# Kernel optimization log

Hardware: AMD Instinct MI355X
Metric: run time of the kernel (lower is better)

## Reference

```python
import jax, jax.numpy as jnp
import numpy as np

N_NODES = 100000


def _degrees(src, dst):
    ones = jnp.ones(src.shape[0], dtype=jnp.float32)
    out_deg = jax.ops.segment_sum(ones, src, num_segments=N_NODES)
    in_deg = jax.ops.segment_sum(ones, dst, num_segments=N_NODES)
    # DGL clamps degrees to a minimum of 1 before the power
    inv_sqrt_out = jax.lax.rsqrt(jnp.maximum(out_deg, 1.0))
    inv_sqrt_in = jax.lax.rsqrt(jnp.maximum(in_deg, 1.0))
    return inv_sqrt_out, inv_sqrt_in


def _graph_conv(h, W, b, src, dst, inv_sqrt_out, inv_sqrt_in):
    # DGL GraphConv, norm='both': D_out^{-1/2} on src feats, SpMM-sum, D_in^{-1/2} on dst
    h = h * inv_sqrt_out[:, None]
    h = h @ W  # applying weight before aggregation is mathematically identical
    agg = jax.ops.segment_sum(h[src], dst, num_segments=N_NODES)
    return agg * inv_sqrt_in[:, None] + b


def setup_inputs() -> dict:
    key = jax.random.key(0)
    ks = jax.random.split(key, 6)
    E, IN, HID = 1600000, 128, 128
    scale = 1.0 / np.sqrt(IN)
    return {
        "feat": jax.random.normal(ks[0], (N_NODES, IN), dtype=jnp.float32),
        "W0": jax.random.normal(ks[1], (IN, HID), dtype=jnp.float32) * scale,
        "b0": jnp.zeros((HID,), dtype=jnp.float32),
        "W1": jax.random.normal(ks[2], (HID, HID), dtype=jnp.float32) * scale,
        "b1": jnp.zeros((HID,), dtype=jnp.float32),
        "W2": jax.random.normal(ks[3], (HID, HID), dtype=jnp.float32) * scale,
        "b2": jnp.zeros((HID,), dtype=jnp.float32),
        "src": jax.random.randint(ks[4], (E,), 0, N_NODES, dtype=jnp.int32),
        "dst": jax.random.randint(ks[5], (E,), 0, N_NODES, dtype=jnp.int32),
    }


def reference(feat, W0, b0, W1, b1, W2, b2, src, dst):
    inv_sqrt_out, inv_sqrt_in = _degrees(src, dst)
    skips = [feat]
    h = feat
    for W, b in ((W0, b0), (W1, b1), (W2, b2)):
        h = jax.nn.relu(_graph_conv(h, W, b, src, dst, inv_sqrt_out, inv_sqrt_in))
        skips.append(h)
    return jnp.concatenate(skips, axis=1)  # torch.hstack on 2D == concat along dim 1
```

## Files before the change

kernel.cpp:

```cpp
#include <hip/hip_runtime.h>
#include <hip/hip_fp16.h>

#define NN 100000
#define NE 1600000
#define FD 128
#define OS 512
#define LDA 136
#define NBKT 196
#define PCH 4096

typedef __attribute__((ext_vector_type(8))) short short8;
typedef __attribute__((ext_vector_type(4))) float f32x4;

__device__ __forceinline__ short f2bf(float x) {
    unsigned u = __float_as_uint(x);
    u = (u + 0x7fff + ((u >> 16) & 1)) >> 16;
    return (short)u;
}

__global__ void k_init_out(const float* __restrict__ feat, float* __restrict__ out) {
    const size_t total = (size_t)NN * 32;
    for (size_t i = (size_t)blockIdx.x * blockDim.x + threadIdx.x; i < total;
         i += (size_t)gridDim.x * blockDim.x) {
        size_t n = i >> 5;
        int c4 = (int)(i & 31);
        ((float4*)(out + n * OS))[c4] = ((const float4*)feat)[n * 32 + c4];
    }
}

__global__ void k_prep_w(const float* __restrict__ W0, const float* __restrict__ W1,
                         const float* __restrict__ W2, short* __restrict__ Wt) {
    int i = blockIdx.x * blockDim.x + threadIdx.x;
    if (i >= 3 * FD * FD) return;
    int l = i >> 14, r = i & (FD * FD - 1);
    int n = r >> 7, k = r & 127;
    const float* W = (l == 0) ? W0 : ((l == 1) ? W1 : W2);
    Wt[i] = f2bf(W[k * FD + n]);
}

__global__ __launch_bounds__(256) void k_deg(const int* __restrict__ src,
                                             const int* __restrict__ dst,
                                             int* __restrict__ cnt_out,
                                             int* __restrict__ bktcnt) {
    __shared__ int h[NBKT];
    for (int i = threadIdx.x; i < NBKT; i += 256) h[i] = 0;
    __syncthreads();
    const int total4 = NE / 4;
    for (int i = blockIdx.x * blockDim.x + threadIdx.x; i < total4;
         i += gridDim.x * blockDim.x) {
        int4 s = ((const int4*)src)[i];
        int4 d = ((const int4*)dst)[i];
        atomicAdd(&cnt_out[s.x], 1); atomicAdd(&cnt_out[s.y], 1);
        atomicAdd(&cnt_out[s.z], 1); atomicAdd(&cnt_out[s.w], 1);
        atomicAdd(&h[d.x >> 9], 1); atomicAdd(&h[d.y >> 9], 1);
        atomicAdd(&h[d.z >> 9], 1); atomicAdd(&h[d.w >> 9], 1);
    }
    __syncthreads();
    for (int i = threadIdx.x; i < NBKT; i += 256)
        if (h[i]) atomicAdd(&bktcnt[i], h[i]);
}

__global__ void k_invsqrt(const int* __restrict__ cnt, float* __restrict__ inv, int n) {
    int i = blockIdx.x * blockDim.x + threadIdx.x;
    if (i < n) inv[i] = rsqrtf((float)max(cnt[i], 1));
}

__global__ __launch_bounds__(256) void k_bkt_scan(const int* __restrict__ bktcnt,
                                                  int* __restrict__ bkt_base,
                                                  int* __restrict__ bkt_cursor) {
    __shared__ int s[256];
    const int tid = threadIdx.x;
    int v = (tid < NBKT) ? bktcnt[tid] : 0;
    s[tid] = v;
    __syncthreads();
    for (int off = 1; off < 256; off <<= 1) {
        int t = (tid >= off) ? s[tid - off] : 0;
        __syncthreads();
        s[tid] += t;
        __syncthreads();
    }
    int excl = s[tid] - v;
    if (tid < NBKT) { bkt_base[tid] = excl; bkt_cursor[tid] = excl; }
    if (tid == NBKT - 1) bkt_base[NBKT] = excl + v;
}

__global__ __launch_bounds__(256) void k_part(const int* __restrict__ src,
                                              const int* __restrict__ dst,
                                              int* __restrict__ bkt_cursor,
                                              int2* __restrict__ pairs) {
    __shared__ int hist[NBKT];
    __shared__ int base[NBKT];
    __shared__ int lofs[NBKT];
    const int tid = threadIdx.x;
    const int e0 = blockIdx.x * PCH;
    for (int i = tid; i < NBKT; i += 256) { hist[i] = 0; lofs[i] = 0; }
    __syncthreads();
    int md[16], ms[16];
    #pragma unroll
    for (int k = 0; k < 16; ++k) {
        int e = e0 + k * 256 + tid;
        md[k] = (e < NE) ? dst[e] : -1;
        ms[k] = (e < NE) ? src[e] : 0;
    }
    #pragma unroll
    for (int k = 0; k < 16; ++k)
        if (md[k] >= 0) atomicAdd(&hist[md[k] >> 9], 1);
    __syncthreads();
    for (int i = tid; i < NBKT; i += 256)
        base[i] = hist[i] ? atomicAdd(&bkt_cursor[i], hist[i]) : 0;
    __syncthreads();
    #pragma unroll
    for (int k = 0; k < 16; ++k)
        if (md[k] >= 0) {
            int b = md[k] >> 9;
            int off = atomicAdd(&lofs[b], 1);
            pairs[base[b] + off] = make_int2(ms[k], md[k]);
        }
}

__global__ __launch_bounds__(256) void k_build(const int2* __restrict__ pairs,
                                               const int* __restrict__ bkt_base,
                                               int* __restrict__ row_ptr,
                                               int* __restrict__ col,
                                               float* __restrict__ inv_in) {
    __shared__ int cnt_s[512];
    __shared__ int wsum[4];
    const int b = blockIdx.x;
    const int tid = threadIdx.x;
    const int lane = tid & 63, wid = tid >> 6;
    const int ebeg = bkt_base[b], eend = bkt_base[b + 1];
    const int n0 = b << 9;
    cnt_s[tid] = 0; cnt_s[tid + 256] = 0;
    __syncthreads();
    for (int e = ebeg + tid; e < eend; e += 256)
        atomicAdd(&cnt_s[pairs[e].y - n0], 1);
    __syncthreads();
    const int v0 = cnt_s[2 * tid], v1 = cnt_s[2 * tid + 1];
    const int sum2 = v0 + v1;
    int incl = sum2;
    #pragma unroll
    for (int off = 1; off < 64; off <<= 1) {
        int t = __shfl_up(incl, off, 64);
        if (lane >= off) incl += t;
    }
    if (lane == 63) wsum[wid] = incl;
    __syncthreads();
    if (tid == 0) {
        int c = 0;
        #pragma unroll
        for (int i = 0; i < 4; ++i) { int t = wsum[i]; wsum[i] = c; c += t; }
    }
    __syncthreads();
    const int e0 = wsum[wid] + incl - sum2;
    cnt_s[2 * tid] = e0;
    cnt_s[2 * tid + 1] = e0 + v0;
    const int g0 = n0 + 2 * tid, g1 = g0 + 1;
    if (g0 < NN) { row_ptr[g0] = ebeg + e0; inv_in[g0] = rsqrtf((float)max(v0, 1)); }
    if (g1 < NN) { row_ptr[g1] = ebeg + e0 + v0; inv_in[g1] = rsqrtf((float)max(v1, 1)); }
    if (b == NBKT - 1 && tid == 0) row_ptr[NN] = eend;
    __syncthreads();
    for (int e = ebeg + tid; e < eend; e += 256) {
        int2 p = pairs[e];
        int pos = atomicAdd(&cnt_s[p.y - n0], 1);
        col[ebeg + pos] = p.x;
    }
}

__global__ __launch_bounds__(256) void k_gemm(const float* __restrict__ h, int hstride,
                                              const short* __restrict__ Wt,
                                              const float* __restrict__ inv_out,
                                              unsigned char* __restrict__ tmp8,
                                              float* __restrict__ scales) {
    __shared__ short Ws[FD * LDA];
    __shared__ short hA[64 * LDA];
    const int tid = threadIdx.x;
    for (int i = tid; i < FD * 16; i += 256) {
        int n = i >> 4, c = i & 15;
        short8 v = *(const short8*)(Wt + n * FD + c * 8);
        *(short8*)(&Ws[n * LDA + c * 8]) = v;
    }
    const int row0 = blockIdx.x * 128;
    const int wid = tid >> 6, lane = tid & 63;
    const int m = lane & 15, quad = lane >> 4;

    for (int sub = 0; sub < 2; ++sub) {
        const int rbase = row0 + sub * 64;
        __syncthreads();
        for (int i = tid; i < 64 * 32; i += 256) {
            int r = i >> 5, c4 = i & 31;
            int gr = rbase + r;
            float4 v = make_float4(0.f, 0.f, 0.f, 0.f);
            if (gr < NN) v = ((const float4*)(h + (size_t)gr * hstride))[c4];
            short4 b;
            b.x = f2bf(v.x); b.y = f2bf(v.y); b.z = f2bf(v.z); b.w = f2bf(v.w);
            *(short4*)(&hA[r * LDA + c4 * 4]) = b;
        }
        __syncthreads();
        const int rtile = rbase + wid * 16;
        short8 a0 = *(const short8*)(&hA[(wid * 16 + m) * LDA + 0 * 32 + quad * 8]);
        short8 a1 = *(const short8*)(&hA[(wid * 16 + m) * LDA + 1 * 32 + quad * 8]);
        short8 a2 = *(const short8*)(&hA[(wid * 16 + m) * LDA + 2 * 32 + quad * 8]);
        short8 a3 = *(const short8*)(&hA[(wid * 16 + m) * LDA + 3 * 32 + quad * 8]);
        float s0, s1, s2, s3;
        {
            int r = rtile + quad * 4;
            s0 = (r + 0 < NN) ? inv_out[r + 0] : 0.f;
            s1 = (r + 1 < NN) ? inv_out[r + 1] : 0.f;
            s2 = (r + 2 < NN) ? inv_out[r + 2] : 0.f;
            s3 = (r + 3 < NN) ? inv_out[r + 3] : 0.f;
        }
        f32x4 accs[8];
        #pragma unroll
        for (int ct = 0; ct < 8; ++ct) {
            f32x4 acc = {0.f, 0.f, 0.f, 0.f};
            short8 b0 = *(const short8*)(&Ws[(ct * 16 + m) * LDA + 0 * 32 + quad * 8]);
            short8 b1 = *(const short8*)(&Ws[(ct * 16 + m) * LDA + 1 * 32 + quad * 8]);
            short8 b2 = *(const short8*)(&Ws[(ct * 16 + m) * LDA + 2 * 32 + quad * 8]);
            short8 b3 = *(const short8*)(&Ws[(ct * 16 + m) * LDA + 3 * 32 + quad * 8]);
            acc = __builtin_amdgcn_mfma_f32_16x16x32_bf16(a0, b0, acc, 0, 0, 0);
            acc = __builtin_amdgcn_mfma_f32_16x16x32_bf16(a1, b1, acc, 0, 0, 0);
            acc = __builtin_amdgcn_mfma_f32_16x16x32_bf16(a2, b2, acc, 0, 0, 0);
            acc = __builtin_amdgcn_mfma_f32_16x16x32_bf16(a3, b3, acc, 0, 0, 0);
            acc[0] *= s0; acc[1] *= s1; acc[2] *= s2; acc[3] *= s3;
            accs[ct] = acc;
        }
        float pm0 = 0.f, pm1 = 0.f, pm2 = 0.f, pm3 = 0.f;
        #pragma unroll
        for (int ct = 0; ct < 8; ++ct) {
            pm0 = fmaxf(pm0, fabsf(accs[ct][0]));
            pm1 = fmaxf(pm1, fabsf(accs[ct][1]));
            pm2 = fmaxf(pm2, fabsf(accs[ct][2]));
            pm3 = fmaxf(pm3, fabsf(accs[ct][3]));
        }
        #pragma unroll
        for (int off = 1; off < 16; off <<= 1) {
            pm0 = fmaxf(pm0, __shfl_xor(pm0, off));
            pm1 = fmaxf(pm1, __shfl_xor(pm1, off));
            pm2 = fmaxf(pm2, __shfl_xor(pm2, off));
            pm3 = fmaxf(pm3, __shfl_xor(pm3, off));
        }
        const float is0 = pm0 > 0.f ? 127.f / pm0 : 0.f;
        const float is1 = pm1 > 0.f ? 127.f / pm1 : 0.f;
        const float is2 = pm2 > 0.f ? 127.f / pm2 : 0.f;
        const float is3 = pm3 > 0.f ? 127.f / pm3 : 0.f;
        const int r = rtile + quad * 4;
        if (m == 0) {
            const float inv127 = 1.f / 127.f;
            if (r + 3 < NN) {
                float4 sv = make_float4(pm0 * inv127, pm1 * inv127, pm2 * inv127, pm3 * inv127);
                *((float4*)(scales + r)) = sv;
            } else {
                if (r + 0 < NN) scales[r + 0] = pm0 * inv127;
                if (r + 1 < NN) scales[r + 1] = pm1 * inv127;
                if (r + 2 < NN) scales[r + 2] = pm2 * inv127;
                if (r + 3 < NN) scales[r + 3] = pm3 * inv127;
            }
        }
        unsigned long long w0 = 0ull, w1 = 0ull, w2 = 0ull, w3 = 0ull;
        #pragma unroll
        for (int ct = 0; ct < 8; ++ct) {
            unsigned char q0 = (unsigned char)(char)(int)rintf(accs[ct][0] * is0);
            unsigned char q1 = (unsigned char)(char)(int)rintf(accs[ct][1] * is1);
            unsigned char q2 = (unsigned char)(char)(int)rintf(accs[ct][2] * is2);
            unsigned char q3 = (unsigned char)(char)(int)rintf(accs[ct][3] * is3);
            w0 |= (unsigned long long)q0 << (8 * ct);
            w1 |= (unsigned long long)q1 << (8 * ct);
            w2 |= (unsigned long long)q2 << (8 * ct);
            w3 |= (unsigned long long)q3 << (8 * ct);
        }
        unsigned char* base = tmp8 + (size_t)r * FD + m * 8;
        if (r + 3 < NN) {
            *(unsigned long long*)(base + 0 * FD) = w0;
            *(unsigned long long*)(base + 1 * FD) = w1;
            *(unsigned long long*)(base + 2 * FD) = w2;
            *(unsigned long long*)(base + 3 * FD) = w3;
        } else {
            if (r + 0 < NN) *(unsigned long long*)(base + 0 * FD) = w0;
            if (r + 1 < NN) *(unsigned long long*)(base + 1 * FD) = w1;
            if (r + 2 < NN) *(unsigned long long*)(base + 2 * FD) = w2;
            if (r + 3 < NN) *(unsigned long long*)(base + 3 * FD) = w3;
        }
    }
}

__global__ __launch_bounds__(256) void k_gather(const unsigned char* __restrict__ tmp8,
                                                const float* __restrict__ scales,
                                                const int* __restrict__ row_ptr,
                                                const int* __restrict__ col,
                                                const float* __restrict__ inv_in,
                                                const float* __restrict__ bias,
                                                float* __restrict__ out, int off) {
    const int wid = threadIdx.x >> 6;
    const int lane = threadIdx.x & 63;
    const int half = lane >> 5;
    const int sl = lane & 31;
    const int node = blockIdx.x * 4 + wid;
    if (node >= NN) return;
    const int beg = row_ptr[node], end = row_ptr[node + 1];
    float a0 = 0.f, a1 = 0.f, a2 = 0.f, a3 = 0.f;
    int j = beg + half;
    for (; j + 6 < end; j += 8) {
        int s0 = col[j], s1 = col[j + 2], s2 = col[j + 4], s3 = col[j + 6];
        char4 c0 = *(const char4*)(tmp8 + (size_t)s0 * FD + sl * 4);
        char4 c1 = *(const char4*)(tmp8 + (size_t)s1 * FD + sl * 4);
        char4 c2 = *(const char4*)(tmp8 + (size_t)s2 * FD + sl * 4);
        char4 c3 = *(const char4*)(tmp8 + (size_t)s3 * FD + sl * 4);
        float f0 = scales[s0], f1 = scales[s1], f2 = scales[s2], f3 = scales[s3];
        a0 += f0 * (float)c0.x + f1 * (float)c1.x + f2 * (float)c2.x + f3 * (float)c3.x;
        a1 += f0 * (float)c0.y + f1 * (float)c1.y + f2 * (float)c2.y + f3 * (float)c3.y;
        a2 += f0 * (float)c0.z + f1 * (float)c1.z + f2 * (float)c2.z + f3 * (float)c3.z;
        a3 += f0 * (float)c0.w + f1 * (float)c1.w + f2 * (float)c2.w + f3 * (float)c3.w;
    }
    for (; j < end; j += 2) {
        int s0 = col[j];
        char4 c0 = *(const char4*)(tmp8 + (size_t)s0 * FD + sl * 4);
        float f0 = scales[s0];
        a0 += f0 * (float)c0.x;
        a1 += f0 * (float)c0.y;
        a2 += f0 * (float)c0.z;
        a3 += f0 * (float)c0.w;
    }
    a0 += __shfl_xor(a0, 32);
    a1 += __shfl_xor(a1, 32);
    a2 += __shfl_xor(a2, 32);
    a3 += __shfl_xor(a3, 32);
    if (half == 0) {
        const float s = inv_in[node];
        float* ob = out + (size_t)node * OS + off;
        float av[4] = {a0, a1, a2, a3};
        #pragma unroll
        for (int k = 0; k < 4; ++k) {
            int jj = 4 * sl + k;
            int c = ((jj & 7) << 4) + (jj >> 3);
            ob[c] = fmaxf(av[k] * s + bias[c], 0.f);
        }
    }
}

extern "C" void kernel_launch(void* const* d_in, const int* in_sizes, int n_in,
                              void* d_out, int out_size, void* d_ws, size_t ws_size,
                              hipStream_t stream) {
    const float* feat = (const float*)d_in[0];
    const float* W0 = (const float*)d_in[1];
    const float* b0 = (const float*)d_in[2];
    const float* W1 = (const float*)d_in[3];
    const float* b1 = (const float*)d_in[4];
    const float* W2 = (const float*)d_in[5];
    const float* b2 = (const float*)d_in[6];
    const int* src = (const int*)d_in[7];
    const int* dst = (const int*)d_in[8];
    float* out = (float*)d_out;
    float* ws = (float*)d_ws;

    unsigned char* tmp8 = (unsigned char*)ws;
    int2* pairs = (int2*)(ws + (size_t)NN * 64);
    float* scales = ws + (size_t)NN * 96;
    float* base2 = ws + (size_t)NN * 128;
    int* cnt_out = (int*)base2;
    int* bktcnt = cnt_out + NN;
    int* bkt_base = bktcnt + NBKT;
    int* bkt_cursor = bkt_base + NBKT + 1;
    float* inv = (float*)(bkt_cursor + NBKT);
    int* row_ptr = (int*)(inv + 2 * NN);
    int* col = row_ptr + NN + 1;
    short* Wt = (short*)(col + NE);

    hipMemsetAsync(cnt_out, 0, (NN + NBKT) * sizeof(int), stream);
    k_init_out<<<4096, 256, 0, stream>>>(feat, out);
    k_prep_w<<<(3 * FD * FD + 255) / 256, 256, 0, stream>>>(W0, W1, W2, Wt);
    k_deg<<<2048, 256, 0, stream>>>(src, dst, cnt_out, bktcnt);
    k_bkt_scan<<<1, 256, 0, stream>>>(bktcnt, bkt_base, bkt_cursor);
    k_part<<<(NE + PCH - 1) / PCH, 256, 0, stream>>>(src, dst, bkt_cursor, pairs);
    k_build<<<NBKT, 256, 0, stream>>>(pairs, bkt_base, row_ptr, col, inv + NN);
    k_invsqrt<<<(NN + 255) / 256, 256, 0, stream>>>(cnt_out, inv, NN);

    const float* bs[3] = {b0, b1, b2};
    const float* h = feat;
    int hstride = FD;
    for (int l = 0; l < 3; ++l) {
        k_gemm<<<(NN + 127) / 128, 256, 0, stream>>>(h, hstride, Wt + l * FD * FD, inv,
                                                     tmp8, scales);
        k_gather<<<(NN + 3) / 4, 256, 0, stream>>>(tmp8, scales, row_ptr, col, inv + NN,
                                                   bs[l], out, FD * (l + 1));
        h = out + FD * (l + 1);
        hstride = OS;
    }
}
```

Baseline: 626.6 us.

## Count out-degrees via src bucket partition and vectorize gather output stores

Replaces the global per-node atomic out-degree count with a bucketed partition of source ids, written as 16-bit local ids, followed by a per-bucket shared-memory histogram. This drops the large memset and the separate invsqrt kernel. The gather epilogue now stages each row in LDS so it can write one float4 per lane instead of four scattered scalar stores. The cost is an extra partition write stream and one more kernel, plus added LDS use in gather.

```diff
diff --git a/kernel.cpp b/kernel.cpp
--- a/kernel.cpp
+++ b/kernel.cpp
@@ -40,81 +40,104 @@
 
 __global__ __launch_bounds__(256) void k_deg(const int* __restrict__ src,
                                              const int* __restrict__ dst,
-                                             int* __restrict__ cnt_out,
-                                             int* __restrict__ bktcnt) {
-    __shared__ int h[NBKT];
-    for (int i = threadIdx.x; i < NBKT; i += 256) h[i] = 0;
+                                             int* __restrict__ bktcnt_d,
+                                             int* __restrict__ bktcnt_s) {
+    __shared__ int hd[NBKT];
+    __shared__ int hs[NBKT];
+    for (int i = threadIdx.x; i < NBKT; i += 256) { hd[i] = 0; hs[i] = 0; }
     __syncthreads();
     const int total4 = NE / 4;
     for (int i = blockIdx.x * blockDim.x + threadIdx.x; i < total4;
          i += gridDim.x * blockDim.x) {
         int4 s = ((const int4*)src)[i];
         int4 d = ((const int4*)dst)[i];
-        atomicAdd(&cnt_out[s.x], 1); atomicAdd(&cnt_out[s.y], 1);
-        atomicAdd(&cnt_out[s.z], 1); atomicAdd(&cnt_out[s.w], 1);
-        atomicAdd(&h[d.x >> 9], 1); atomicAdd(&h[d.y >> 9], 1);
-        atomicAdd(&h[d.z >> 9], 1); atomicAdd(&h[d.w >> 9], 1);
-    }
-    __syncthreads();
-    for (int i = threadIdx.x; i < NBKT; i += 256)
-        if (h[i]) atomicAdd(&bktcnt[i], h[i]);
-}
-
-__global__ void k_invsqrt(const int* __restrict__ cnt, float* __restrict__ inv, int n) {
-    int i = blockIdx.x * blockDim.x + threadIdx.x;
-    if (i < n) inv[i] = rsqrtf((float)max(cnt[i], 1));
-}
-
-__global__ __launch_bounds__(256) void k_bkt_scan(const int* __restrict__ bktcnt,
-                                                  int* __restrict__ bkt_base,
-                                                  int* __restrict__ bkt_cursor) {
-    __shared__ int s[256];
+        atomicAdd(&hs[s.x >> 9], 1); atomicAdd(&hs[s.y >> 9], 1);
+        atomicAdd(&hs[s.z >> 9], 1); atomicAdd(&hs[s.w >> 9], 1);
+        atomicAdd(&hd[d.x >> 9], 1); atomicAdd(&hd[d.y >> 9], 1);
+        atomicAdd(&hd[d.z >> 9], 1); atomicAdd(&hd[d.w >> 9], 1);
+    }
+    __syncthreads();
+    for (int i = threadIdx.x; i < NBKT; i += 256) {
+        if (hd[i]) atomicAdd(&bktcnt_d[i], hd[i]);
+        if (hs[i]) atomicAdd(&bktcnt_s[i], hs[i]);
+    }
+}
+
+__global__ __launch_bounds__(256) void k_scan2(const int* __restrict__ bktcnt_d,
+                                               const int* __restrict__ bktcnt_s,
+                                               int* __restrict__ base_d,
+                                               int* __restrict__ cur_d,
+                                               int* __restrict__ base_s,
+                                               int* __restrict__ cur_s) {
+    __shared__ int sh[256];
     const int tid = threadIdx.x;
-    int v = (tid < NBKT) ? bktcnt[tid] : 0;
-    s[tid] = v;
+    int v = (tid < NBKT) ? bktcnt_d[tid] : 0;
+    sh[tid] = v;
     __syncthreads();
     for (int off = 1; off < 256; off <<= 1) {
-        int t = (tid >= off) ? s[tid - off] : 0;
-        __syncthreads();
-        s[tid] += t;
-        __syncthreads();
-    }
-    int excl = s[tid] - v;
-    if (tid < NBKT) { bkt_base[tid] = excl; bkt_cursor[tid] = excl; }
-    if (tid == NBKT - 1) bkt_base[NBKT] = excl + v;
+        int t = (tid >= off) ? sh[tid - off] : 0;
+        __syncthreads();
+        sh[tid] += t;
+        __syncthreads();
+    }
+    int excl = sh[tid] - v;
+    if (tid < NBKT) { base_d[tid] = excl; cur_d[tid] = excl; }
+    if (tid == NBKT - 1) base_d[NBKT] = excl + v;
+    __syncthreads();
+    v = (tid < NBKT) ? bktcnt_s[tid] : 0;
+    sh[tid] = v;
+    __syncthreads();
+    for (int off = 1; off < 256; off <<= 1) {
+        int t = (tid >= off) ? sh[tid - off] : 0;
+        __syncthreads();
+        sh[tid] += t;
+        __syncthreads();
+    }
+    excl = sh[tid] - v;
+    if (tid < NBKT) { base_s[tid] = excl; cur_s[tid] = excl; }
+    if (tid == NBKT - 1) base_s[NBKT] = excl + v;
 }
 
 __global__ __launch_bounds__(256) void k_part(const int* __restrict__ src,
                                               const int* __restrict__ dst,
-                                              int* __restrict__ bkt_cursor,
-                                              int2* __restrict__ pairs) {
-    __shared__ int hist[NBKT];
-    __shared__ int base[NBKT];
-    __shared__ int lofs[NBKT];
+                                              int* __restrict__ cur_d,
+                                              int* __restrict__ cur_s,
+                                              int2* __restrict__ pairs,
+                                              unsigned short* __restrict__ ssrc) {
+    __shared__ int hd[NBKT], bd[NBKT], ld_[NBKT];
+    __shared__ int hs_[NBKT], bs_[NBKT], ls_[NBKT];
     const int tid = threadIdx.x;
     const int e0 = blockIdx.x * PCH;
-    for (int i = tid; i < NBKT; i += 256) { hist[i] = 0; lofs[i] = 0; }
+    for (int i = tid; i < NBKT; i += 256) { hd[i] = 0; ld_[i] = 0; hs_[i] = 0; ls_[i] = 0; }
     __syncthreads();
     int md[16], ms[16];
     #pragma unroll
     for (int k = 0; k < 16; ++k) {
         int e = e0 + k * 256 + tid;
         md[k] = (e < NE) ? dst[e] : -1;
-        ms[k] = (e < NE) ? src[e] : 0;
+        ms[k] = (e < NE) ? src[e] : -1;
     }
     #pragma unroll
     for (int k = 0; k < 16; ++k)
-        if (md[k] >= 0) atomicAdd(&hist[md[k] >> 9], 1);
-    __syncthreads();
-    for (int i = tid; i < NBKT; i += 256)
-        base[i] = hist[i] ? atomicAdd(&bkt_cursor[i], hist[i]) : 0;
+        if (md[k] >= 0) {
+            atomicAdd(&hd[md[k] >> 9], 1);
+            atomicAdd(&hs_[ms[k] >> 9], 1);
+        }
+    __syncthreads();
+    for (int i = tid; i < NBKT; i += 256) {
+        bd[i] = hd[i] ? atomicAdd(&cur_d[i], hd[i]) : 0;
+        bs_[i] = hs_[i] ? atomicAdd(&cur_s[i], hs_[i]) : 0;
+    }
     __syncthreads();
     #pragma unroll
     for (int k = 0; k < 16; ++k)
         if (md[k] >= 0) {
             int b = md[k] >> 9;
-            int off = atomicAdd(&lofs[b], 1);
-            pairs[base[b] + off] = make_int2(ms[k], md[k]);
+            int off = atomicAdd(&ld_[b], 1);
+            pairs[bd[b] + off] = make_int2(ms[k], md[k]);
+            int b2 = ms[k] >> 9;
+            int off2 = atomicAdd(&ls_[b2], 1);
+            ssrc[bs_[b2] + off2] = (unsigned short)(ms[k] & 511);
         }
 }
 
@@ -164,6 +187,24 @@
         int pos = atomicAdd(&cnt_s[p.y - n0], 1);
         col[ebeg + pos] = p.x;
     }
+}
+
+__global__ __launch_bounds__(256) void k_build_src(const unsigned short* __restrict__ ssrc,
+                                                   const int* __restrict__ base_s,
+                                                   float* __restrict__ inv_out) {
+    __shared__ int cnt_s[512];
+    const int b = blockIdx.x;
+    const int tid = threadIdx.x;
+    const int ebeg = base_s[b], eend = base_s[b + 1];
+    cnt_s[tid] = 0; cnt_s[tid + 256] = 0;
+    __syncthreads();
+    for (int e = ebeg + tid; e < eend; e += 256)
+        atomicAdd(&cnt_s[ssrc[e]], 1);
+    __syncthreads();
+    const int n0 = b << 9;
+    const int g0 = n0 + tid, g1 = g0 + 256;
+    if (g0 < NN) inv_out[g0] = rsqrtf((float)max(cnt_s[tid], 1));
+    if (g1 < NN) inv_out[g1] = rsqrtf((float)max(cnt_s[tid + 256], 1));
 }
 
 __global__ __launch_bounds__(256) void k_gemm(const float* __restrict__ h, int hstride,
@@ -290,6 +331,7 @@
                                                 const float* __restrict__ inv_in,
                                                 const float* __restrict__ bias,
                                                 float* __restrict__ out, int off) {
+    __shared__ float ob_s[4][128];
     const int wid = threadIdx.x >> 6;
     const int lane = threadIdx.x & 63;
     const int half = lane >> 5;
@@ -325,15 +367,22 @@
     a2 += __shfl_xor(a2, 32);
     a3 += __shfl_xor(a3, 32);
     if (half == 0) {
-        const float s = inv_in[node];
-        float* ob = out + (size_t)node * OS + off;
         float av[4] = {a0, a1, a2, a3};
         #pragma unroll
         for (int k = 0; k < 4; ++k) {
             int jj = 4 * sl + k;
             int c = ((jj & 7) << 4) + (jj >> 3);
-            ob[c] = fmaxf(av[k] * s + bias[c], 0.f);
-        }
+            ob_s[wid][c] = av[k];
+        }
+        const float s = inv_in[node];
+        float4 f4 = ((const float4*)ob_s[wid])[sl];
+        const float4 bb = ((const float4*)bias)[sl];
+        float4 r;
+        r.x = fmaxf(f4.x * s + bb.x, 0.f);
+        r.y = fmaxf(f4.y * s + bb.y, 0.f);
+        r.z = fmaxf(f4.z * s + bb.z, 0.f);
+        r.w = fmaxf(f4.w * s + bb.w, 0.f);
+        ((float4*)(out + (size_t)node * OS + off))[sl] = r;
     }
 }
 
@@ -355,24 +404,27 @@
     unsigned char* tmp8 = (unsigned char*)ws;
     int2* pairs = (int2*)(ws + (size_t)NN * 64);
     float* scales = ws + (size_t)NN * 96;
-    float* base2 = ws + (size_t)NN * 128;
-    int* cnt_out = (int*)base2;
-    int* bktcnt = cnt_out + NN;
-    int* bkt_base = bktcnt + NBKT;
-    int* bkt_cursor = bkt_base + NBKT + 1;
-    float* inv = (float*)(bkt_cursor + NBKT);
+    unsigned short* ssrc = (unsigned short*)(ws + (size_t)NN * 104);
+    int* base2 = (int*)(ws + (size_t)NN * 128);
+    int* bktcnt_d = base2;
+    int* bktcnt_s = bktcnt_d + NBKT;
+    int* base_d = bktcnt_s + NBKT;
+    int* cur_d = base_d + NBKT + 1;
+    int* base_s = cur_d + NBKT;
+    int* cur_s = base_s + NBKT + 1;
+    float* inv = (float*)(cur_s + NBKT);
     int* row_ptr = (int*)(inv + 2 * NN);
     int* col = row_ptr + NN + 1;
     short* Wt = (short*)(col + NE);
 
-    hipMemsetAsync(cnt_out, 0, (NN + NBKT) * sizeof(int), stream);
+    hipMemsetAsync(bktcnt_d, 0, 2 * NBKT * sizeof(int), stream);
     k_init_out<<<4096, 256, 0, stream>>>(feat, out);
     k_prep_w<<<(3 * FD * FD + 255) / 256, 256, 0, stream>>>(W0, W1, W2, Wt);
-    k_deg<<<2048, 256, 0, stream>>>(src, dst, cnt_out, bktcnt);
-    k_bkt_scan<<<1, 256, 0, stream>>>(bktcnt, bkt_base, bkt_cursor);
-    k_part<<<(NE + PCH - 1) / PCH, 256, 0, stream>>>(src, dst, bkt_cursor, pairs);
-    k_build<<<NBKT, 256, 0, stream>>>(pairs, bkt_base, row_ptr, col, inv + NN);
-    k_invsqrt<<<(NN + 255) / 256, 256, 0, stream>>>(cnt_out, inv, NN);
+    k_deg<<<512, 256, 0, stream>>>(src, dst, bktcnt_d, bktcnt_s);
+    k_scan2<<<1, 256, 0, stream>>>(bktcnt_d, bktcnt_s, base_d, cur_d, base_s, cur_s);
+    k_part<<<(NE + PCH - 1) / PCH, 256, 0, stream>>>(src, dst, cur_d, cur_s, pairs, ssrc);
+    k_build<<<NBKT, 256, 0, stream>>>(pairs, base_d, row_ptr, col, inv + NN);
+    k_build_src<<<NBKT, 256, 0, stream>>>(ssrc, base_s, inv);
 
     const float* bs[3] = {b0, b1, b2};
     const float* h = feat;
```

Result: faster. 566.0 us (-9.7%).
